# Optimization experiments

Measured on AMD Instinct MI355X. Metric: run time of the kernel, lower is better.

Reference implementation:

```python
import jax, jax.numpy as jnp
import numpy as np

GRID_LON = 17  # idx = lat*17 + lon in original code


def setup_inputs() -> dict:
    key = jax.random.key(0)
    ks = jax.random.split(key, 16)
    B, S, L = 512, 256, 64
    DIM_RHO, DIM_C, HID = 256, 128, 512
    N_LAT, N_LON = 17, GRID_LON

    rho = jax.random.normal(ks[0], (B, S, DIM_RHO), dtype=jnp.float32)
    c = jax.random.normal(ks[1], (1, DIM_C, N_LAT, N_LON), dtype=jnp.float32)
    w = jax.random.uniform(ks[2], (B, S), dtype=jnp.float32, minval=1e-3, maxval=1.0)
    l = jax.random.uniform(ks[3], (B,), dtype=jnp.float32, minval=0.1, maxval=10.0)
    roads = jax.random.randint(ks[4], (B, L), 0, N_LAT * N_LON)
    lon_idx = jax.random.randint(ks[5], (B, L), 0, N_LON)
    lat_idx = jax.random.randint(ks[6], (B, L), 0, N_LAT)

    sc = lambda fan_in: 1.0 / np.sqrt(fan_in)
    # f2: MLP(128, 256, 128) with selu
    f2_W1 = jax.random.uniform(ks[7], (DIM_C, 256), jnp.float32, -sc(DIM_C), sc(DIM_C))
    f2_b1 = jnp.zeros((256,), jnp.float32)
    f2_W2 = jax.random.uniform(ks[8], (256, DIM_C), jnp.float32, -sc(256), sc(256))
    f2_b2 = jnp.zeros((DIM_C,), jnp.float32)
    # f: MLP2(dim_rho + dim_c, hidden, 1) with selu (use_selu=True)
    fin = DIM_RHO + DIM_C
    f_W1 = jax.random.uniform(ks[9], (fin, HID), jnp.float32, -sc(fin), sc(fin))
    f_b1 = jnp.zeros((HID,), jnp.float32)
    f_W21 = jax.random.uniform(ks[10], (HID, 1), jnp.float32, -sc(HID), sc(HID))
    f_b21 = jnp.zeros((1,), jnp.float32)
    f_W22 = jax.random.uniform(ks[11], (HID, 1), jnp.float32, -sc(HID), sc(HID))
    f_b22 = jnp.zeros((1,), jnp.float32)

    return dict(rho=rho, c=c, w=w, l=l, roads=roads, lon_idx=lon_idx,
                lat_idx=lat_idx, f2_W1=f2_W1, f2_b1=f2_b1, f2_W2=f2_W2,
                f2_b2=f2_b2, f_W1=f_W1, f_b1=f_b1, f_W21=f_W21, f_b21=f_b21,
                f_W22=f_W22, f_b22=f_b22)


def reference(rho, c, w, l, roads, lon_idx, lat_idx,
              f2_W1, f2_b1, f2_W2, f2_b2,
              f_W1, f_b1, f_W21, f_b21, f_W22, f_b22):
    # c: (1, dim_c, n_lat, n_lon) -> (n_lat*n_lon, dim_c)
    c3 = jnp.squeeze(c, 0)                       # (dim_c, n_lat, n_lon)
    c_flat = jnp.transpose(c3, (1, 2, 0)).reshape(-1, c3.shape[0])  # (cells, dim_c)

    # ragged gather-mean, vectorized: (B, L) cell indices -> (B, dim_c)
    idx = lat_idx * GRID_LON + lon_idx           # (B, L)
    c_traj = jnp.mean(c_flat[idx], axis=1)       # (B, dim_c)

    # f2: selu MLP (dropout inactive / eval mode)
    h = jax.nn.selu(c_traj @ f2_W1 + f2_b1)
    c_tr = h @ f2_W2 + f2_b2                     # (B, dim_c)

    # broadcast over seq and concat with rho
    S = rho.shape[1]
    c_exp = jnp.broadcast_to(c_tr[:, None, :], (rho.shape[0], S, c_tr.shape[-1]))
    x = jnp.concatenate([rho, c_exp], axis=2)    # (B, S, dim_rho + dim_c)

    # f (MLP2, selu since use_selu=True)
    h1 = jax.nn.selu(x @ f_W1 + f_b1)            # (B, S, hidden)
    logm = (h1 @ f_W21 + f_b21)[..., 0]          # (B, S)
    logv = (h1 @ f_W22 + f_b22)[..., 0]          # (B, S)

    logw = jnp.log(w)
    logm_agg = jax.nn.logsumexp(logm + logw, axis=1)       # (B,)
    logv_agg = jax.nn.logsumexp(logv + 2.0 * logw, axis=1) # (B,)
    logl = jnp.log(l)
    log_mu = logl - logm_agg
    log_lambda = logl - 3.0 * logm_agg - logv_agg
    return (log_mu, log_lambda)
```

## Files before the change

### kernel.cpp

```cpp
#include <hip/hip_runtime.h>
#include <hip/hip_bf16.h>

typedef short bf16x8 __attribute__((ext_vector_type(8)));
typedef float f32x4 __attribute__((ext_vector_type(4)));

__device__ __forceinline__ short f2bf(float f) {
    union { float f; unsigned u; } v; v.f = f;
    unsigned r = (v.u + 0x7FFFu + ((v.u >> 16) & 1u)) >> 16;
    return (short)r;
}

__device__ __forceinline__ float selu_f(float x) {
    const float scale = 1.0507009873554805f;
    const float sa = 1.0507009873554805f * 1.6732632423543772f;
    return x > 0.f ? scale * x : sa * (__expf(x) - 1.f);
}

__global__ void __launch_bounds__(512) prep_cbias_kernel(
    const float* __restrict__ c, const int* __restrict__ lat_idx,
    const int* __restrict__ lon_idx,
    const float* __restrict__ f2W1, const float* __restrict__ f2b1,
    const float* __restrict__ f2W2, const float* __restrict__ f2b2,
    const float* __restrict__ fW1, const float* __restrict__ fb1,
    float* __restrict__ cbias)
{
    __shared__ int cells[64];
    __shared__ float ctraj[128];
    __shared__ float hbuf[256];
    __shared__ float ctrf[128];
    const int b = blockIdx.x;
    const int t = threadIdx.x;

    if (t < 64) cells[t] = lat_idx[b * 64 + t] * 17 + lon_idx[b * 64 + t];
    __syncthreads();

    if (t < 128) {
        float s = 0.f;
        #pragma unroll 8
        for (int j = 0; j < 64; ++j) s += c[t * 289 + cells[j]];
        ctraj[t] = s * (1.f / 64.f);
    }
    __syncthreads();

    if (t < 256) {
        float acc = f2b1[t];
        #pragma unroll 8
        for (int i = 0; i < 128; ++i) acc += ctraj[i] * f2W1[i * 256 + t];
        hbuf[t] = selu_f(acc);
    }
    __syncthreads();

    if (t < 128) {
        float acc = f2b2[t];
        #pragma unroll 8
        for (int i = 0; i < 256; ++i) acc += hbuf[i] * f2W2[i * 128 + t];
        ctrf[t] = acc;
    }
    __syncthreads();

    float acc = fb1[t];
    #pragma unroll 8
    for (int i = 0; i < 128; ++i) acc += ctrf[i] * fW1[(256 + i) * 512 + t];
    cbias[b * 512 + t] = acc;
}

__global__ void __launch_bounds__(256) build_w1img_kernel(
    const float* __restrict__ fW1, short* __restrict__ img)
{
    int I = blockIdx.x * 256 + threadIdx.x;
    int e = I & 7;
    int lane = (I >> 3) & 63;
    int cg = (I >> 9) & 31;
    int kc = I >> 14;
    int col = cg * 16 + (lane & 15);
    int k = kc * 32 + ((lane >> 4) << 3) + e;
    img[I] = f2bf(fW1[k * 512 + col]);
}

__global__ void __launch_bounds__(256, 2) fused_gemm_kernel(
    const float* __restrict__ rho, const short* __restrict__ w1img,
    const float* __restrict__ cbias, const float* __restrict__ fw21,
    const float* __restrict__ fw22,
    float* __restrict__ plm, float* __restrict__ plv)
{
    __shared__ __align__(16) char smA[32768];
    __shared__ float redM[4][64];
    __shared__ float redV[4][64];

    const int tid  = threadIdx.x;
    const int lane = tid & 63;
    const int w    = tid >> 6;
    const int l15  = lane & 15;
    const int hi   = lane >> 4;

    const int b  = blockIdx.x >> 2;
    const int s0 = (blockIdx.x & 3) << 6;

    {
        const float* rbase = rho + (size_t)(b * 256 + s0) * 256;
        const int row  = ((tid >> 6) << 4) + (tid & 15);
        const int kseg = (tid >> 4) & 3;
        const float* src = rbase + (size_t)row * 256 + kseg * 8;
        #pragma unroll
        for (int i = 0; i < 8; ++i) {
            float4 f0 = *(const float4*)(src + i * 32);
            float4 f1 = *(const float4*)(src + i * 32 + 4);
            bf16x8 h;
            h[0] = f2bf(f0.x); h[1] = f2bf(f0.y); h[2] = f2bf(f0.z); h[3] = f2bf(f0.w);
            h[4] = f2bf(f1.x); h[5] = f2bf(f1.y); h[6] = f2bf(f1.z); h[7] = f2bf(f1.w);
            *(bf16x8*)(smA + (i * 256 + tid) * 16) = h;
        }
    }
    __syncthreads();

    f32x4 acc[4][8];
    #pragma unroll
    for (int rf = 0; rf < 4; ++rf)
        #pragma unroll
        for (int cf = 0; cf < 8; ++cf)
            acc[rf][cf] = (f32x4){0.f, 0.f, 0.f, 0.f};

    const char* bimg = (const char*)w1img + (size_t)w * 8192 + lane * 16;

    #pragma unroll
    for (int kc = 0; kc < 8; ++kc) {
        bf16x8 aF[4];
        #pragma unroll
        for (int rf = 0; rf < 4; ++rf)
            aF[rf] = *(const bf16x8*)(smA + ((kc * 4 + rf) * 64 + lane) * 16);
        bf16x8 bF[8];
        #pragma unroll
        for (int cf = 0; cf < 8; ++cf)
            bF[cf] = *(const bf16x8*)(bimg + (size_t)kc * 32768 + cf * 1024);
        #pragma unroll
        for (int rf = 0; rf < 4; ++rf)
            #pragma unroll
            for (int cf = 0; cf < 8; ++cf)
                acc[rf][cf] = __builtin_amdgcn_mfma_f32_16x16x32_bf16(
                    aF[rf], bF[cf], acc[rf][cf], 0, 0, 0);
    }

    float cb[8], w21r[8], w22r[8];
    #pragma unroll
    for (int cf = 0; cf < 8; ++cf) {
        int col = w * 128 + cf * 16 + l15;
        cb[cf]   = cbias[b * 512 + col];
        w21r[cf] = fw21[col];
        w22r[cf] = fw22[col];
    }

    #pragma unroll
    for (int rf = 0; rf < 4; ++rf)
        #pragma unroll
        for (int q = 0; q < 4; ++q) {
            float m = 0.f, v = 0.f;
            #pragma unroll
            for (int cf = 0; cf < 8; ++cf) {
                float s_ = selu_f(acc[rf][cf][q] + cb[cf]);
                m += s_ * w21r[cf];
                v += s_ * w22r[cf];
            }
            #pragma unroll
            for (int d = 1; d < 16; d <<= 1) {
                m += __shfl_xor(m, d);
                v += __shfl_xor(v, d);
            }
            if (l15 == 0) {
                int row = rf * 16 + hi * 4 + q;
                redM[w][row] = m;
                redV[w][row] = v;
            }
        }

    __syncthreads();
    size_t obase = (size_t)b * 256 + s0;
    if (tid < 64) {
        plm[obase + tid] = redM[0][tid] + redM[1][tid] + redM[2][tid] + redM[3][tid];
    } else if (tid < 128) {
        int rr = tid - 64;
        plv[obase + rr] = redV[0][rr] + redV[1][rr] + redV[2][rr] + redV[3][rr];
    }
}

__global__ void __launch_bounds__(64) finalize_kernel(
    const float* __restrict__ plm, const float* __restrict__ plv,
    const float* __restrict__ w, const float* __restrict__ l,
    const float* __restrict__ b21p, const float* __restrict__ b22p,
    float* __restrict__ out)
{
    const int b = blockIdx.x;
    const int lane = threadIdx.x;
    const float b21 = b21p[0], b22 = b22p[0];

    float a1[4], a2[4];
    float m1 = -1e30f, m2 = -1e30f;
    #pragma unroll
    for (int i = 0; i < 4; ++i) {
        int s = i * 64 + lane;
        float lw = logf(w[b * 256 + s]);
        a1[i] = plm[b * 256 + s] + b21 + lw;
        a2[i] = plv[b * 256 + s] + b22 + 2.f * lw;
        m1 = fmaxf(m1, a1[i]);
        m2 = fmaxf(m2, a2[i]);
    }
    #pragma unroll
    for (int m = 1; m < 64; m <<= 1) {
        m1 = fmaxf(m1, __shfl_xor(m1, m));
        m2 = fmaxf(m2, __shfl_xor(m2, m));
    }
    float s1 = 0.f, s2 = 0.f;
    #pragma unroll
    for (int i = 0; i < 4; ++i) {
        s1 += expf(a1[i] - m1);
        s2 += expf(a2[i] - m2);
    }
    #pragma unroll
    for (int m = 1; m < 64; m <<= 1) {
        s1 += __shfl_xor(s1, m);
        s2 += __shfl_xor(s2, m);
    }
    if (lane == 0) {
        float lm_agg = m1 + logf(s1);
        float lv_agg = m2 + logf(s2);
        float logl = logf(l[b]);
        out[b]       = logl - lm_agg;
        out[512 + b] = logl - 3.f * lm_agg - lv_agg;
    }
}

extern "C" void kernel_launch(void* const* d_in, const int* in_sizes, int n_in,
                              void* d_out, int out_size, void* d_ws, size_t ws_size,
                              hipStream_t stream) {
    const float* rho     = (const float*)d_in[0];
    const float* c       = (const float*)d_in[1];
    const float* w       = (const float*)d_in[2];
    const float* l       = (const float*)d_in[3];
    const int*   lon_idx = (const int*)d_in[5];
    const int*   lat_idx = (const int*)d_in[6];
    const float* f2W1    = (const float*)d_in[7];
    const float* f2b1    = (const float*)d_in[8];
    const float* f2W2    = (const float*)d_in[9];
    const float* f2b2    = (const float*)d_in[10];
    const float* fW1     = (const float*)d_in[11];
    const float* fb1     = (const float*)d_in[12];
    const float* fW21    = (const float*)d_in[13];
    const float* fb21    = (const float*)d_in[14];
    const float* fW22    = (const float*)d_in[15];
    const float* fb22    = (const float*)d_in[16];
    float* out = (float*)d_out;

    char* ws = (char*)d_ws;
    float* cbias  = (float*)(ws);
    short* w1img  = (short*)(ws + 1048576);
    float* plm    = (float*)(ws + 1310720);
    float* plv    = (float*)(ws + 1835008);

    prep_cbias_kernel<<<512, 512, 0, stream>>>(c, lat_idx, lon_idx,
                                               f2W1, f2b1, f2W2, f2b2,
                                               fW1, fb1, cbias);
    build_w1img_kernel<<<512, 256, 0, stream>>>(fW1, w1img);
    fused_gemm_kernel<<<2048, 256, 0, stream>>>(rho, w1img, cbias, fW21, fW22,
                                                plm, plv);
    finalize_kernel<<<512, 64, 0, stream>>>(plm, plv, w, l, fb21, fb22, out);
}
```

Measured before the change: 109.7 us.

## Split fused GEMM across 8 waves with 64 columns each and prefetch B

The fused GEMM block grows from 256 to 512 threads, and each wave now covers 64 hidden columns instead of 128, which halves the accumulator registers per wave. The B fragments for the next k-chunk are loaded one step ahead so global loads overlap the MFMAs, and the rho staging is remapped for 512 threads. The final reduction sums partials from 8 waves. This trades more waves per block, and possibly higher occupancy, for extra shared-memory reduction work. The block also loads more of the B image per block, and occupancy is limited by launch bounds (512,4) and 32KB of LDS.

```diff
diff --git a/kernel.cpp b/kernel.cpp
--- a/kernel.cpp
+++ b/kernel.cpp
@@ -77,15 +77,15 @@
     img[I] = f2bf(fW1[k * 512 + col]);
 }
 
-__global__ void __launch_bounds__(256, 2) fused_gemm_kernel(
+__global__ void __launch_bounds__(512, 4) fused_gemm_kernel(
     const float* __restrict__ rho, const short* __restrict__ w1img,
     const float* __restrict__ cbias, const float* __restrict__ fw21,
     const float* __restrict__ fw22,
     float* __restrict__ plm, float* __restrict__ plv)
 {
     __shared__ __align__(16) char smA[32768];
-    __shared__ float redM[4][64];
-    __shared__ float redV[4][64];
+    __shared__ float redM[8][64];
+    __shared__ float redV[8][64];
 
     const int tid  = threadIdx.x;
     const int lane = tid & 63;
@@ -94,56 +94,71 @@
     const int hi   = lane >> 4;
 
     const int b  = blockIdx.x >> 2;
-    const int s0 = (blockIdx.x & 3) << 6;
+    const int s0 = (blockIdx.x & 2) << 5 | (blockIdx.x & 1) << 6;
+    const int s0v = (blockIdx.x & 3) << 6;
 
     {
-        const float* rbase = rho + (size_t)(b * 256 + s0) * 256;
-        const int row  = ((tid >> 6) << 4) + (tid & 15);
-        const int kseg = (tid >> 4) & 3;
-        const float* src = rbase + (size_t)row * 256 + kseg * 8;
-        #pragma unroll
-        for (int i = 0; i < 8; ++i) {
-            float4 f0 = *(const float4*)(src + i * 32);
-            float4 f1 = *(const float4*)(src + i * 32 + 4);
+        const float* rbase = rho + (size_t)(b * 256 + s0v) * 256;
+        #pragma unroll
+        for (int i = 0; i < 4; ++i) {
+            int slot = i * 512 + tid;
+            int kc = slot >> 8;
+            int rem = slot & 255;
+            int rg = rem >> 6;
+            int ls = rem & 63;
+            int row = rg * 16 + (ls & 15);
+            int k0 = kc * 32 + ((ls >> 4) << 3);
+            const float* src = rbase + (size_t)row * 256 + k0;
+            float4 f0 = *(const float4*)(src);
+            float4 f1 = *(const float4*)(src + 4);
             bf16x8 h;
             h[0] = f2bf(f0.x); h[1] = f2bf(f0.y); h[2] = f2bf(f0.z); h[3] = f2bf(f0.w);
             h[4] = f2bf(f1.x); h[5] = f2bf(f1.y); h[6] = f2bf(f1.z); h[7] = f2bf(f1.w);
-            *(bf16x8*)(smA + (i * 256 + tid) * 16) = h;
+            *(bf16x8*)(smA + slot * 16) = h;
         }
     }
     __syncthreads();
 
-    f32x4 acc[4][8];
+    f32x4 acc[4][4];
     #pragma unroll
     for (int rf = 0; rf < 4; ++rf)
         #pragma unroll
-        for (int cf = 0; cf < 8; ++cf)
+        for (int cf = 0; cf < 4; ++cf)
             acc[rf][cf] = (f32x4){0.f, 0.f, 0.f, 0.f};
 
-    const char* bimg = (const char*)w1img + (size_t)w * 8192 + lane * 16;
+    const char* bp = (const char*)w1img + w * 4096 + lane * 16;
+
+    bf16x8 bN[4];
+    #pragma unroll
+    for (int cf = 0; cf < 4; ++cf)
+        bN[cf] = *(const bf16x8*)(bp + cf * 1024);
 
     #pragma unroll
     for (int kc = 0; kc < 8; ++kc) {
+        bf16x8 bC[4];
+        #pragma unroll
+        for (int cf = 0; cf < 4; ++cf) bC[cf] = bN[cf];
+        if (kc < 7) {
+            #pragma unroll
+            for (int cf = 0; cf < 4; ++cf)
+                bN[cf] = *(const bf16x8*)(bp + (size_t)(kc + 1) * 32768 + cf * 1024);
+        }
         bf16x8 aF[4];
         #pragma unroll
         for (int rf = 0; rf < 4; ++rf)
             aF[rf] = *(const bf16x8*)(smA + ((kc * 4 + rf) * 64 + lane) * 16);
-        bf16x8 bF[8];
-        #pragma unroll
-        for (int cf = 0; cf < 8; ++cf)
-            bF[cf] = *(const bf16x8*)(bimg + (size_t)kc * 32768 + cf * 1024);
         #pragma unroll
         for (int rf = 0; rf < 4; ++rf)
             #pragma unroll
-            for (int cf = 0; cf < 8; ++cf)
+            for (int cf = 0; cf < 4; ++cf)
                 acc[rf][cf] = __builtin_amdgcn_mfma_f32_16x16x32_bf16(
-                    aF[rf], bF[cf], acc[rf][cf], 0, 0, 0);
-    }
-
-    float cb[8], w21r[8], w22r[8];
-    #pragma unroll
-    for (int cf = 0; cf < 8; ++cf) {
-        int col = w * 128 + cf * 16 + l15;
+                    aF[rf], bC[cf], acc[rf][cf], 0, 0, 0);
+    }
+
+    float cb[4], w21r[4], w22r[4];
+    #pragma unroll
+    for (int cf = 0; cf < 4; ++cf) {
+        int col = w * 64 + cf * 16 + l15;
         cb[cf]   = cbias[b * 512 + col];
         w21r[cf] = fw21[col];
         w22r[cf] = fw22[col];
@@ -155,7 +170,7 @@
         for (int q = 0; q < 4; ++q) {
             float m = 0.f, v = 0.f;
             #pragma unroll
-            for (int cf = 0; cf < 8; ++cf) {
+            for (int cf = 0; cf < 4; ++cf) {
                 float s_ = selu_f(acc[rf][cf][q] + cb[cf]);
                 m += s_ * w21r[cf];
                 v += s_ * w22r[cf];
@@ -173,12 +188,18 @@
         }
 
     __syncthreads();
-    size_t obase = (size_t)b * 256 + s0;
+    size_t obase = (size_t)b * 256 + s0v;
     if (tid < 64) {
-        plm[obase + tid] = redM[0][tid] + redM[1][tid] + redM[2][tid] + redM[3][tid];
+        float s = 0.f;
+        #pragma unroll
+        for (int j = 0; j < 8; ++j) s += redM[j][tid];
+        plm[obase + tid] = s;
     } else if (tid < 128) {
         int rr = tid - 64;
-        plv[obase + rr] = redV[0][rr] + redV[1][rr] + redV[2][rr] + redV[3][rr];
+        float s = 0.f;
+        #pragma unroll
+        for (int j = 0; j < 8; ++j) s += redV[j][rr];
+        plv[obase + rr] = s;
     }
 }
 
@@ -259,7 +280,7 @@
                                                f2W1, f2b1, f2W2, f2b2,
                                                fW1, fb1, cbias);
     build_w1img_kernel<<<512, 256, 0, stream>>>(fW1, w1img);
-    fused_gemm_kernel<<<2048, 256, 0, stream>>>(rho, w1img, cbias, fW21, fW22,
+    fused_gemm_kernel<<<2048, 512, 0, stream>>>(rho, w1img, cbias, fW21, fW22,
                                                 plm, plv);
     finalize_kernel<<<512, 64, 0, stream>>>(plm, plv, w, l, fb21, fb22, out);
 }
```

Result: faster. 106.0 us (-3.4%).
